# Kernel tuning notes

Hardware: AMD Instinct MI355X
Metric: run time of the kernel (lower is better)

Reference implementation:

```python
import jax, jax.numpy as jnp
import numpy as np
from jax import lax

B, N, C = 16, 16384, 256
NP, NS = 128, 16        # num_proposal, nsample
R = 0.3                 # ball radius (normalize_xyz divides by R)


def setup_inputs() -> dict:
    key = jax.random.key(0)
    ks = jax.random.split(key, 11)
    f32 = jnp.float32
    return dict(
        vote_xyz=jax.random.uniform(ks[0], (B, N, 3), f32),
        vote_features=jax.random.normal(ks[1], (B, C, N), f32),
        # SA shared-MLP 1x1 conv weights (bias folded into BN), mlp=[259,128,128,128]
        W1=jax.random.normal(ks[2], (128, C + 3), f32) * 0.05,
        W2=jax.random.normal(ks[3], (128, 128), f32) * 0.05,
        W3=jax.random.normal(ks[4], (128, 128), f32) * 0.05,
        sa_bn_scale=jax.random.uniform(ks[5], (3, 128), f32, 0.5, 1.5),
        sa_bn_bias=jax.random.normal(ks[6], (3, 128), f32) * 0.1,
        # trailing mlp_module: two Conv1d(128,128,1)+BN(eval)+ReLU
        Wm=jax.random.normal(ks[7], (2, 128, 128), f32) * 0.05,
        bm=jax.random.normal(ks[8], (2, 128), f32) * 0.01,
        m_bn_scale=jax.random.uniform(ks[9], (2, 128), f32, 0.5, 1.5),
        m_bn_bias=jax.random.normal(ks[10], (2, 128), f32) * 0.1,
    )


def _fps(xyz):
    # farthest point sampling, one cloud: xyz [N,3] -> inds [NP]
    def body(carry, _):
        mind, last = carry
        d = jnp.sum((xyz - xyz[last]) ** 2, axis=-1)
        mind = jnp.minimum(mind, d)
        nxt = jnp.argmax(mind).astype(jnp.int32)
        return (mind, nxt), nxt
    init = (jnp.full((xyz.shape[0],), 1e10, xyz.dtype), jnp.int32(0))
    _, rest = lax.scan(body, init, None, length=NP - 1)
    return jnp.concatenate([jnp.zeros((1,), jnp.int32), rest])


def _ball_query(xyz, centers):
    # xyz [N,3], centers [NP,3] -> idx [NP,NS]; first NS in-ball points in
    # original order, padded with the first in-ball index (pointnet2 semantics)
    d2 = jnp.sum((centers[:, None, :] - xyz[None, :, :]) ** 2, axis=-1)  # [NP,N]
    n = xyz.shape[0]
    cand = jnp.where(d2 < R * R, jnp.arange(n, dtype=jnp.int32), jnp.int32(n))
    firstk = jnp.sort(cand, axis=-1)[:, :NS]                             # [NP,NS]
    first = firstk[:, :1]
    idx = jnp.where(firstk == n, first, firstk)
    return jnp.where(idx == n, 0, idx)


def _forward(vote_xyz, vote_features, W1, W2, W3, sa_bn_scale, sa_bn_bias,
             Wm, bm, m_bn_scale, m_bn_bias):
    fps_inds = jax.vmap(_fps)(vote_xyz)                                   # [B,NP]
    new_xyz = jnp.take_along_axis(vote_xyz, fps_inds[..., None], axis=1)  # [B,NP,3]
    idx = jax.vmap(_ball_query)(vote_xyz, new_xyz)                        # [B,NP,NS]
    grouped_xyz = jax.vmap(lambda p, i: p[i])(vote_xyz, idx)              # [B,NP,NS,3]
    grouped_xyz = (grouped_xyz - new_xyz[:, :, None, :]) / R              # normalize_xyz
    grouped_feat = jax.vmap(lambda f, i: f[:, i])(vote_features, idx)     # [B,C,NP,NS]
    g = jnp.concatenate([grouped_xyz.transpose(0, 3, 1, 2), grouped_feat], axis=1)  # [B,C+3,NP,NS]
    for W, s, b in ((W1, sa_bn_scale[0], sa_bn_bias[0]),
                    (W2, sa_bn_scale[1], sa_bn_bias[1]),
                    (W3, sa_bn_scale[2], sa_bn_bias[2])):
        g = jax.nn.relu(jnp.einsum('bcsn,oc->bosn', g, W)
                        * s[None, :, None, None] + b[None, :, None, None])
    feat = jnp.max(g, axis=-1)                                            # [B,128,NP] max pool
    for k in range(2):
        feat = jax.nn.relu((jnp.einsum('bcs,oc->bos', feat, Wm[k]) + bm[k][None, :, None])
                           * m_bn_scale[k][None, :, None] + m_bn_bias[k][None, :, None])
    return new_xyz, feat, fps_inds


def reference(vote_xyz, vote_features, W1, W2, W3, sa_bn_scale, sa_bn_bias,
              Wm, bm, m_bn_scale, m_bn_bias):
    return _forward(vote_xyz, vote_features, W1, W2, W3, sa_bn_scale, sa_bn_bias,
                    Wm, bm, m_bn_scale, m_bn_bias)
```

## Files before the change

### kernel.cpp

```cpp
#include <hip/hip_runtime.h>
#include <hip/hip_bf16.h>

#define NB  16
#define NN  16384
#define NC  256
#define NPP 128
#define NSS 16

#define FTH 1024

__global__ __launch_bounds__(256) void transpose_kernel(
    const float* __restrict__ W1, const float* __restrict__ W2,
    const float* __restrict__ W3, const float* __restrict__ Wm,
    float* __restrict__ W1T, float* __restrict__ W2T,
    float* __restrict__ W3T, float* __restrict__ WmT) {
  int i = blockIdx.x * 256 + threadIdx.x;
  if (i < 128 * 259) { int o = i / 259, c = i - o * 259; W1T[c * 128 + o] = W1[i]; }
  if (i < 128 * 128) {
    int o = i >> 7, c = i & 127;
    W2T[c * 128 + o] = W2[i];
    W3T[c * 128 + o] = W3[i];
    WmT[c * 128 + o] = Wm[i];
    WmT[16384 + c * 128 + o] = Wm[16384 + i];
  }
}

__global__ __attribute__((amdgpu_flat_work_group_size(1024, 1024)))
void fps_kernel(
    const float* __restrict__ xyz,
    float* __restrict__ centers, float* __restrict__ out_xyz,
    float* __restrict__ out_indf) {
  int b = blockIdx.x;
  const float* px = xyz + (size_t)b * (NN * 3);
  int t = threadIdx.x;
  __shared__ float2 sxy[NN / 2];
  __shared__ unsigned long long cand[2][16];
  __shared__ float4 hist[NPP];
  float Xr[8], Yr[8], Zr[16], MD[16];
#pragma unroll
  for (int j = 0; j < 16; ++j) {
    int n = t + (j << 10);
    float x = px[n * 3 + 0];
    float y = px[n * 3 + 1];
    float z = px[n * 3 + 2];
    asm volatile("" : "+v"(z));
    if (j < 8) {
      asm volatile("" : "+v"(x), "+v"(y));
      Xr[j] = x; Yr[j] = y;
    } else {
      sxy[n - 8192] = make_float2(x, y);
    }
    Zr[j] = z;
    MD[j] = 1e10f;
  }
  float cx = px[0], cy = px[1], cz = px[2];
  if (t == 0) hist[0] = make_float4(cx, cy, cz, 0.0f);
  __syncthreads();
  for (int it = 1; it < NPP; ++it) {
    float bv = -1.0f;
    int bi = 0;
#pragma unroll
    for (int j = 0; j < 8; ++j) {
      float dx = __fsub_rn(Xr[j], cx);
      float dy = __fsub_rn(Yr[j], cy);
      float dz = __fsub_rn(Zr[j], cz);
      float d  = __fadd_rn(__fadd_rn(__fmul_rn(dx, dx), __fmul_rn(dy, dy)),
                           __fmul_rn(dz, dz));
      float m = fminf(MD[j], d);
      MD[j] = m;
      if (m > bv) { bv = m; bi = t + (j << 10); }
    }
#pragma unroll
    for (int j = 8; j < 16; ++j) {
      float2 v = sxy[t + ((j - 8) << 10)];
      float dx = __fsub_rn(v.x, cx);
      float dy = __fsub_rn(v.y, cy);
      float dz = __fsub_rn(Zr[j], cz);
      float d  = __fadd_rn(__fadd_rn(__fmul_rn(dx, dx), __fmul_rn(dy, dy)),
                           __fmul_rn(dz, dz));
      float m = fminf(MD[j], d);
      MD[j] = m;
      if (m > bv) { bv = m; bi = t + (j << 10); }
    }
    unsigned long long pk =
        (((unsigned long long)__float_as_uint(bv)) << 32) |
        (unsigned long long)(~(unsigned)bi);
#define STEP_ROR(N)                                                         \
    {                                                                       \
      unsigned lo = (unsigned)pk, hi = (unsigned)(pk >> 32);                \
      lo = (unsigned)__builtin_amdgcn_mov_dpp((int)lo, 0x120 | N, 0xF, 0xF, true); \
      hi = (unsigned)__builtin_amdgcn_mov_dpp((int)hi, 0x120 | N, 0xF, 0xF, true); \
      unsigned long long o = ((unsigned long long)hi << 32) | lo;           \
      if (o > pk) pk = o;                                                   \
    }
    STEP_ROR(1) STEP_ROR(2) STEP_ROR(4) STEP_ROR(8)
    {
      unsigned lo = (unsigned)pk, hi = (unsigned)(pk >> 32);
      lo = (unsigned)__builtin_amdgcn_ds_swizzle((int)lo, 0x401F);
      hi = (unsigned)__builtin_amdgcn_ds_swizzle((int)hi, 0x401F);
      unsigned long long o = ((unsigned long long)hi << 32) | lo;
      if (o > pk) pk = o;
    }
    {
      unsigned long long o = __shfl_xor(pk, 32, 64);
      if (o > pk) pk = o;
    }
    int p = it & 1;
    if ((t & 63) == 0) cand[p][t >> 6] = pk;
    __syncthreads();
    pk = cand[p][t & 15];
    STEP_ROR(1) STEP_ROR(2) STEP_ROR(4) STEP_ROR(8)
#undef STEP_ROR
    int win = (int)(~(unsigned)(pk & 0xFFFFFFFFull));
    win = __builtin_amdgcn_readfirstlane(win);
    cx = px[win * 3 + 0];
    cy = px[win * 3 + 1];
    cz = px[win * 3 + 2];
    if (t == 0) hist[it] = make_float4(cx, cy, cz, (float)win);
  }
  __syncthreads();
  if (t < NPP) {
    float4 h = hist[t];
    centers[(b * NPP + t) * 3 + 0] = h.x;
    centers[(b * NPP + t) * 3 + 1] = h.y;
    centers[(b * NPP + t) * 3 + 2] = h.z;
    out_xyz[(b * NPP + t) * 3 + 0] = h.x;
    out_xyz[(b * NPP + t) * 3 + 1] = h.y;
    out_xyz[(b * NPP + t) * 3 + 2] = h.z;
    out_indf[b * NPP + t] = h.w;
  }
}

__global__ __launch_bounds__(64) void ballq_kernel(
    const float* __restrict__ xyz, const float* __restrict__ centers,
    int* __restrict__ bidx) {
  int bs = blockIdx.x;
  int b = bs >> 7;
  int lane = threadIdx.x;
  const float* px = xyz + (size_t)b * (NN * 3);
  float cx = centers[bs * 3 + 0];
  float cy = centers[bs * 3 + 1];
  float cz = centers[bs * 3 + 2];
  __shared__ int coll[NSS];
  const float rr = 0.09f;
  int have = 0;
  for (int c0 = 0; c0 < NN; c0 += 64) {
    int n = c0 + lane;
    float dx = __fsub_rn(px[n * 3 + 0], cx);
    float dy = __fsub_rn(px[n * 3 + 1], cy);
    float dz = __fsub_rn(px[n * 3 + 2], cz);
    float d2 = __fadd_rn(__fadd_rn(__fmul_rn(dx, dx), __fmul_rn(dy, dy)),
                         __fmul_rn(dz, dz));
    bool in = d2 < rr;
    unsigned long long m = __ballot(in);
    if (in) {
      int pos = have + __popcll(m & ((1ull << lane) - 1ull));
      if (pos < NSS) coll[pos] = n;
    }
    have += __popcll(m);
    if (have >= NSS) break;
  }
  __syncthreads();
  int first = coll[0];
  if (lane < NSS) bidx[bs * NSS + lane] = (lane < have) ? coll[lane] : first;
}

__device__ __forceinline__ float4 bnrelu4(float4 a, float s, float b) {
  float4 r;
  r.x = fmaxf(fmaf(a.x, s, b), 0.f);
  r.y = fmaxf(fmaf(a.y, s, b), 0.f);
  r.z = fmaxf(fmaf(a.z, s, b), 0.f);
  r.w = fmaxf(fmaf(a.w, s, b), 0.f);
  return r;
}

__device__ __forceinline__ void layer4(const float (*in)[20], int cin,
                                       const float* __restrict__ WT,
                                       const float* __restrict__ sc,
                                       const float* __restrict__ bi,
                                       int o4, int k0,
                                       float4& r0, float4& r1,
                                       float4& r2, float4& r3) {
  float4 a0 = {0.f, 0.f, 0.f, 0.f}, a1 = a0, a2 = a0, a3 = a0;
  for (int c = 0; c < cin; ++c) {
    float4 w  = *(const float4*)(WT + c * 128 + o4);
    float4 gv = *(const float4*)(&in[c][k0]);
    a0.x = fmaf(w.x, gv.x, a0.x); a0.y = fmaf(w.x, gv.y, a0.y);
    a0.z = fmaf(w.x, gv.z, a0.z); a0.w = fmaf(w.x, gv.w, a0.w);
    a1.x = fmaf(w.y, gv.x, a1.x); a1.y = fmaf(w.y, gv.y, a1.y);
    a1.z = fmaf(w.y, gv.z, a1.z); a1.w = fmaf(w.y, gv.w, a1.w);
    a2.x = fmaf(w.z, gv.x, a2.x); a2.y = fmaf(w.z, gv.y, a2.y);
    a2.z = fmaf(w.z, gv.z, a2.z); a2.w = fmaf(w.z, gv.w, a2.w);
    a3.x = fmaf(w.w, gv.x, a3.x); a3.y = fmaf(w.w, gv.y, a3.y);
    a3.z = fmaf(w.w, gv.z, a3.z); a3.w = fmaf(w.w, gv.w, a3.w);
  }
  r0 = bnrelu4(a0, sc[o4 + 0], bi[o4 + 0]);
  r1 = bnrelu4(a1, sc[o4 + 1], bi[o4 + 1]);
  r2 = bnrelu4(a2, sc[o4 + 2], bi[o4 + 2]);
  r3 = bnrelu4(a3, sc[o4 + 3], bi[o4 + 3]);
}

__global__ __launch_bounds__(128) void mlp_kernel(
    const float* __restrict__ xyz, const float* __restrict__ feats,
    const float* __restrict__ centers, const int* __restrict__ bidx,
    const float* __restrict__ W1T, const float* __restrict__ W2T,
    const float* __restrict__ W3T, const float* __restrict__ sa_sc,
    const float* __restrict__ sa_bi, float* __restrict__ feat0) {
  int bs = blockIdx.x;
  int b = bs >> 7;
  int s = bs & 127;
  int tid = threadIdx.x;
  __shared__ __align__(16) float g[259][20];
  __shared__ __align__(16) float h1[128][20];
  float (*h2)[20] = (float (*)[20]) & g[0][0];
  __shared__ int kidx[NSS];
  __shared__ float ctr[3];
  if (tid < NSS) kidx[tid] = bidx[bs * NSS + tid];
  if (tid < 3) ctr[tid] = centers[bs * 3 + tid];
  __syncthreads();
  const float* px = xyz + (size_t)b * (NN * 3);
  if (tid < NSS) {
    int n = kidx[tid];
    g[0][tid] = __fdiv_rn(__fsub_rn(px[n * 3 + 0], ctr[0]), 0.3f);
    g[1][tid] = __fdiv_rn(__fsub_rn(px[n * 3 + 1], ctr[1]), 0.3f);
    g[2][tid] = __fdiv_rn(__fsub_rn(px[n * 3 + 2], ctr[2]), 0.3f);
  }
#pragma unroll
  for (int cc = 0; cc < 2; ++cc) {
    int c = tid + cc * 128;
    const float* row = feats + ((size_t)b * NC + c) * NN;
#pragma unroll
    for (int k = 0; k < NSS; ++k) g[3 + c][k] = row[kidx[k]];
  }
  __syncthreads();
  int o4 = (tid & 31) * 4;
  int k0 = (tid >> 5) * 4;
  float4 r0, r1, r2, r3;
  layer4(g, 259, W1T, sa_sc, sa_bi, o4, k0, r0, r1, r2, r3);
  *(float4*)&h1[o4 + 0][k0] = r0;
  *(float4*)&h1[o4 + 1][k0] = r1;
  *(float4*)&h1[o4 + 2][k0] = r2;
  *(float4*)&h1[o4 + 3][k0] = r3;
  __syncthreads();
  layer4(h1, 128, W2T, sa_sc + 128, sa_bi + 128, o4, k0, r0, r1, r2, r3);
  __syncthreads();
  *(float4*)&h2[o4 + 0][k0] = r0;
  *(float4*)&h2[o4 + 1][k0] = r1;
  *(float4*)&h2[o4 + 2][k0] = r2;
  *(float4*)&h2[o4 + 3][k0] = r3;
  __syncthreads();
  layer4(h2, 128, W3T, sa_sc + 256, sa_bi + 256, o4, k0, r0, r1, r2, r3);
  float m0 = fmaxf(fmaxf(r0.x, r0.y), fmaxf(r0.z, r0.w));
  float m1 = fmaxf(fmaxf(r1.x, r1.y), fmaxf(r1.z, r1.w));
  float m2 = fmaxf(fmaxf(r2.x, r2.y), fmaxf(r2.z, r2.w));
  float m3 = fmaxf(fmaxf(r3.x, r3.y), fmaxf(r3.z, r3.w));
  int kg = tid >> 5;
  h1[o4 + 0][kg] = m0;
  h1[o4 + 1][kg] = m1;
  h1[o4 + 2][kg] = m2;
  h1[o4 + 3][kg] = m3;
  __syncthreads();
  if (tid < 128) {
    float m = fmaxf(fmaxf(h1[tid][0], h1[tid][1]), fmaxf(h1[tid][2], h1[tid][3]));
    feat0[((size_t)b * 128 + tid) * 128 + s] = m;
  }
}

__global__ __launch_bounds__(256) void head_kernel(
    const float* __restrict__ feat0, const float* __restrict__ WmT,
    const float* __restrict__ bm, const float* __restrict__ msc,
    const float* __restrict__ mbi, float* __restrict__ out_feat) {
  int blk = blockIdx.x;
  int b = blk >> 2;
  int sbase = (blk & 3) * 32;
  int tid = threadIdx.x;
  __shared__ float fa[128][36];
  __shared__ float fb[128][36];
  {
    int sj = tid & 31, c0 = tid >> 5;
    for (int c = c0; c < 128; c += 8)
      fa[c][sj] = feat0[((size_t)b * 128 + c) * 128 + sbase + sj];
  }
  __syncthreads();
  int o2 = (tid & 63) * 2, s0 = (tid >> 6) * 8;
  float a0[8], a1[8];
#pragma unroll
  for (int j = 0; j < 8; ++j) { a0[j] = 0.f; a1[j] = 0.f; }
  for (int c = 0; c < 128; ++c) {
    float2 w = *(const float2*)&WmT[c * 128 + o2];
    float4 f0 = *(const float4*)&fa[c][s0];
    float4 f1 = *(const float4*)&fa[c][s0 + 4];
    a0[0] = fmaf(w.x, f0.x, a0[0]); a0[1] = fmaf(w.x, f0.y, a0[1]);
    a0[2] = fmaf(w.x, f0.z, a0[2]); a0[3] = fmaf(w.x, f0.w, a0[3]);
    a0[4] = fmaf(w.x, f1.x, a0[4]); a0[5] = fmaf(w.x, f1.y, a0[5]);
    a0[6] = fmaf(w.x, f1.z, a0[6]); a0[7] = fmaf(w.x, f1.w, a0[7]);
    a1[0] = fmaf(w.y, f0.x, a1[0]); a1[1] = fmaf(w.y, f0.y, a1[1]);
    a1[2] = fmaf(w.y, f0.z, a1[2]); a1[3] = fmaf(w.y, f0.w, a1[3]);
    a1[4] = fmaf(w.y, f1.x, a1[4]); a1[5] = fmaf(w.y, f1.y, a1[5]);
    a1[6] = fmaf(w.y, f1.z, a1[6]); a1[7] = fmaf(w.y, f1.w, a1[7]);
  }
  {
    float c0 = bm[o2], c1 = bm[o2 + 1];
    float t0 = msc[o2], t1 = msc[o2 + 1];
    float q0 = mbi[o2], q1 = mbi[o2 + 1];
#pragma unroll
    for (int j = 0; j < 8; ++j) {
      fb[o2][s0 + j]     = fmaxf(fmaf(a0[j] + c0, t0, q0), 0.f);
      fb[o2 + 1][s0 + j] = fmaxf(fmaf(a1[j] + c1, t1, q1), 0.f);
    }
  }
  __syncthreads();
#pragma unroll
  for (int j = 0; j < 8; ++j) { a0[j] = 0.f; a1[j] = 0.f; }
  for (int c = 0; c < 128; ++c) {
    float2 w = *(const float2*)&WmT[16384 + c * 128 + o2];
    float4 f0 = *(const float4*)&fb[c][s0];
    float4 f1 = *(const float4*)&fb[c][s0 + 4];
    a0[0] = fmaf(w.x, f0.x, a0[0]); a0[1] = fmaf(w.x, f0.y, a0[1]);
    a0[2] = fmaf(w.x, f0.z, a0[2]); a0[3] = fmaf(w.x, f0.w, a0[3]);
    a0[4] = fmaf(w.x, f1.x, a0[4]); a0[5] = fmaf(w.x, f1.y, a0[5]);
    a0[6] = fmaf(w.x, f1.z, a0[6]); a0[7] = fmaf(w.x, f1.w, a0[7]);
    a1[0] = fmaf(w.y, f0.x, a1[0]); a1[1] = fmaf(w.y, f0.y, a1[1]);
    a1[2] = fmaf(w.y, f0.z, a1[2]); a1[3] = fmaf(w.y, f0.w, a1[3]);
    a1[4] = fmaf(w.y, f1.x, a1[4]); a1[5] = fmaf(w.y, f1.y, a1[5]);
    a1[6] = fmaf(w.y, f1.z, a1[6]); a1[7] = fmaf(w.y, f1.w, a1[7]);
  }
  {
    float c0 = bm[128 + o2], c1 = bm[128 + o2 + 1];
    float t0 = msc[128 + o2], t1 = msc[128 + o2 + 1];
    float q0 = mbi[128 + o2], q1 = mbi[128 + o2 + 1];
    float4 v0a, v0b, v1a, v1b;
    v0a.x = fmaxf(fmaf(a0[0] + c0, t0, q0), 0.f);
    v0a.y = fmaxf(fmaf(a0[1] + c0, t0, q0), 0.f);
    v0a.z = fmaxf(fmaf(a0[2] + c0, t0, q0), 0.f);
    v0a.w = fmaxf(fmaf(a0[3] + c0, t0, q0), 0.f);
    v0b.x = fmaxf(fmaf(a0[4] + c0, t0, q0), 0.f);
    v0b.y = fmaxf(fmaf(a0[5] + c0, t0, q0), 0.f);
    v0b.z = fmaxf(fmaf(a0[6] + c0, t0, q0), 0.f);
    v0b.w = fmaxf(fmaf(a0[7] + c0, t0, q0), 0.f);
    v1a.x = fmaxf(fmaf(a1[0] + c1, t1, q1), 0.f);
    v1a.y = fmaxf(fmaf(a1[1] + c1, t1, q1), 0.f);
    v1a.z = fmaxf(fmaf(a1[2] + c1, t1, q1), 0.f);
    v1a.w = fmaxf(fmaf(a1[3] + c1, t1, q1), 0.f);
    v1b.x = fmaxf(fmaf(a1[4] + c1, t1, q1), 0.f);
    v1b.y = fmaxf(fmaf(a1[5] + c1, t1, q1), 0.f);
    v1b.z = fmaxf(fmaf(a1[6] + c1, t1, q1), 0.f);
    v1b.w = fmaxf(fmaf(a1[7] + c1, t1, q1), 0.f);
    float* p0 = &out_feat[((size_t)b * 128 + o2) * 128 + sbase + s0];
    float* p1 = &out_feat[((size_t)b * 128 + o2 + 1) * 128 + sbase + s0];
    *(float4*)p0 = v0a;
    *(float4*)(p0 + 4) = v0b;
    *(float4*)p1 = v1a;
    *(float4*)(p1 + 4) = v1b;
  }
}

extern "C" void kernel_launch(void* const* d_in, const int* in_sizes, int n_in,
                              void* d_out, int out_size, void* d_ws, size_t ws_size,
                              hipStream_t stream) {
  const float* vote_xyz  = (const float*)d_in[0];
  const float* vote_feat = (const float*)d_in[1];
  const float* W1   = (const float*)d_in[2];
  const float* W2   = (const float*)d_in[3];
  const float* W3   = (const float*)d_in[4];
  const float* sasc = (const float*)d_in[5];
  const float* sabi = (const float*)d_in[6];
  const float* Wm   = (const float*)d_in[7];
  const float* bm   = (const float*)d_in[8];
  const float* msc  = (const float*)d_in[9];
  const float* mbi  = (const float*)d_in[10];

  float* out = (float*)d_out;
  float* out_xyz  = out;
  float* out_feat = out + 6144;
  float* out_indf = out + 6144 + 262144;

  char* ws = (char*)d_ws;
  float* centers = (float*)(ws + 8192);
  int*   bidx    = (int*)(ws + 32768);
  float* W1T     = (float*)(ws + 163840);
  float* W2T     = (float*)(ws + 296448);
  float* W3T     = (float*)(ws + 361984);
  float* WmT     = (float*)(ws + 427520);
  float* feat0   = (float*)(ws + 558592);

  hipLaunchKernelGGL(transpose_kernel, dim3(130), dim3(256), 0, stream,
                     W1, W2, W3, Wm, W1T, W2T, W3T, WmT);
  hipLaunchKernelGGL(fps_kernel, dim3(NB), dim3(FTH), 0, stream,
                     vote_xyz, centers, out_xyz, out_indf);
  hipLaunchKernelGGL(ballq_kernel, dim3(NB * NPP), dim3(64), 0, stream,
                     vote_xyz, centers, bidx);
  hipLaunchKernelGGL(mlp_kernel, dim3(NB * NPP), dim3(128), 0, stream,
                     vote_xyz, vote_feat, centers, bidx, W1T, W2T, W3T,
                     sasc, sabi, feat0);
  hipLaunchKernelGGL(head_kernel, dim3(NB * 4), dim3(256), 0, stream,
                     feat0, WmT, bm, msc, mbi, out_feat);
}
```

Before: 362.1 us.

## Keep all FPS xy in LDS as point pairs and fetch winner from LDS

```diff
diff --git a/kernel.cpp b/kernel.cpp
--- a/kernel.cpp
+++ b/kernel.cpp
@@ -33,54 +33,54 @@
   int b = blockIdx.x;
   const float* px = xyz + (size_t)b * (NN * 3);
   int t = threadIdx.x;
-  __shared__ float2 sxy[NN / 2];
+  __shared__ __align__(16) float4 sxy4[NN / 2];
   __shared__ unsigned long long cand[2][16];
+  __shared__ float zcand[2][16];
   __shared__ float4 hist[NPP];
-  float Xr[8], Yr[8], Zr[16], MD[16];
-#pragma unroll
-  for (int j = 0; j < 16; ++j) {
-    int n = t + (j << 10);
-    float x = px[n * 3 + 0];
-    float y = px[n * 3 + 1];
-    float z = px[n * 3 + 2];
-    asm volatile("" : "+v"(z));
-    if (j < 8) {
-      asm volatile("" : "+v"(x), "+v"(y));
-      Xr[j] = x; Yr[j] = y;
-    } else {
-      sxy[n - 8192] = make_float2(x, y);
-    }
-    Zr[j] = z;
-    MD[j] = 1e10f;
+  float Zr[16], MD[16];
+#pragma unroll
+  for (int q = 0; q < 8; ++q) {
+    int pq = t + (q << 10);
+    const float* p = px + pq * 6;
+    float x0 = p[0], y0 = p[1], z0 = p[2];
+    float x1 = p[3], y1 = p[4], z1 = p[5];
+    asm volatile("" : "+v"(z0), "+v"(z1));
+    sxy4[pq] = make_float4(x0, y0, x1, y1);
+    Zr[2 * q] = z0; Zr[2 * q + 1] = z1;
+    MD[2 * q] = 1e10f; MD[2 * q + 1] = 1e10f;
   }
   float cx = px[0], cy = px[1], cz = px[2];
   if (t == 0) hist[0] = make_float4(cx, cy, cz, 0.0f);
   __syncthreads();
   for (int it = 1; it < NPP; ++it) {
-    float bv = -1.0f;
+    float bv = -1.0f, bz = 0.0f;
     int bi = 0;
-#pragma unroll
-    for (int j = 0; j < 8; ++j) {
-      float dx = __fsub_rn(Xr[j], cx);
-      float dy = __fsub_rn(Yr[j], cy);
-      float dz = __fsub_rn(Zr[j], cz);
-      float d  = __fadd_rn(__fadd_rn(__fmul_rn(dx, dx), __fmul_rn(dy, dy)),
-                           __fmul_rn(dz, dz));
-      float m = fminf(MD[j], d);
-      MD[j] = m;
-      if (m > bv) { bv = m; bi = t + (j << 10); }
-    }
-#pragma unroll
-    for (int j = 8; j < 16; ++j) {
-      float2 v = sxy[t + ((j - 8) << 10)];
-      float dx = __fsub_rn(v.x, cx);
-      float dy = __fsub_rn(v.y, cy);
-      float dz = __fsub_rn(Zr[j], cz);
-      float d  = __fadd_rn(__fadd_rn(__fmul_rn(dx, dx), __fmul_rn(dy, dy)),
-                           __fmul_rn(dz, dz));
-      float m = fminf(MD[j], d);
-      MD[j] = m;
-      if (m > bv) { bv = m; bi = t + (j << 10); }
+    float4 nxt = sxy4[t];
+#pragma unroll
+    for (int q = 0; q < 8; ++q) {
+      float4 v = nxt;
+      if (q < 7) nxt = sxy4[t + ((q + 1) << 10)];
+      int n0 = 2 * t + (q << 11);
+      {
+        float dx = __fsub_rn(v.x, cx);
+        float dy = __fsub_rn(v.y, cy);
+        float dz = __fsub_rn(Zr[2 * q], cz);
+        float d  = __fadd_rn(__fadd_rn(__fmul_rn(dx, dx), __fmul_rn(dy, dy)),
+                             __fmul_rn(dz, dz));
+        float m = fminf(MD[2 * q], d);
+        MD[2 * q] = m;
+        if (m > bv) { bv = m; bi = n0; bz = Zr[2 * q]; }
+      }
+      {
+        float dx = __fsub_rn(v.z, cx);
+        float dy = __fsub_rn(v.w, cy);
+        float dz = __fsub_rn(Zr[2 * q + 1], cz);
+        float d  = __fadd_rn(__fadd_rn(__fmul_rn(dx, dx), __fmul_rn(dy, dy)),
+                             __fmul_rn(dz, dz));
+        float m = fminf(MD[2 * q + 1], d);
+        MD[2 * q + 1] = m;
+        if (m > bv) { bv = m; bi = n0 + 1; bz = Zr[2 * q + 1]; }
+      }
     }
     unsigned long long pk =
         (((unsigned long long)__float_as_uint(bv)) << 32) |
@@ -106,6 +106,8 @@
       if (o > pk) pk = o;
     }
     int p = it & 1;
+    int widx = (int)(~(unsigned)(pk & 0xFFFFFFFFull));
+    if (bi == widx) zcand[p][t >> 6] = bz;
     if ((t & 63) == 0) cand[p][t >> 6] = pk;
     __syncthreads();
     pk = cand[p][t & 15];
@@ -113,9 +115,10 @@
 #undef STEP_ROR
     int win = (int)(~(unsigned)(pk & 0xFFFFFFFFull));
     win = __builtin_amdgcn_readfirstlane(win);
-    cx = px[win * 3 + 0];
-    cy = px[win * 3 + 1];
-    cz = px[win * 3 + 2];
+    cz = zcand[p][((win >> 1) & 1023) >> 6];
+    float4 wv = sxy4[win >> 1];
+    cx = (win & 1) ? wv.z : wv.x;
+    cy = (win & 1) ? wv.w : wv.y;
     if (t == 0) hist[it] = make_float4(cx, cy, cz, (float)win);
   }
   __syncthreads();
```

Result: slower. 378.0 us (+4.4%).
